# Performance work log

Hardware: AMD Instinct MI355X
Metric: run time of the kernel (lower is better)

The kernel has to match this reference:

```python
import jax, jax.numpy as jnp
import numpy as np

H, B, S, D, T = 4, 16, 2048, 128, 5  # n_head, batch, seq_len, d_model, num event types
BAND_K = 64  # latest-k band width, as in get_latest_k_mask


def setup_inputs() -> dict:
    key = jax.random.key(0)
    ks = jax.random.split(key, 5)
    output = jax.random.normal(ks[0], (B, S, D), dtype=jnp.float32)
    # banded 'latest-k' mask: mask[i, i:i+k] = 1  (start=max(i,i-k+1)=i, end=min(S,i+k))
    i = jnp.arange(S)
    band = ((i[None, :] >= i[:, None]) & (i[None, :] < i[:, None] + BAND_K)).astype(jnp.float32)
    local_cor = band[None]  # [1, S, S]
    cor_matrix = jax.random.normal(ks[1], (T, D), dtype=jnp.float32)
    event_type = jax.random.randint(ks[2], (B, S), 1, T + 1)  # 1-based event ids in [1, T]
    # per-head linear3 params (xavier-ish); self.linear is unused in forward
    W3 = jax.random.normal(ks[3], (H, D, D), dtype=jnp.float32) / np.sqrt(D)
    b3 = jnp.zeros((H, D), dtype=jnp.float32)
    return dict(output=output, local_cor=local_cor, cor_matrix=cor_matrix,
                event_type=event_type, W3=W3, b3=b3)


def reference(output, local_cor, cor_matrix, event_type, W3, b3):
    # (corr^T @ cor_matrix[et-1]).mean(2) == einsum('bsd,bs->bd', corr, cor_matrix[et-1].mean(-1))
    g = cor_matrix.mean(-1)[event_type - 1]  # [B, S]
    x = output
    sum_seq = jnp.zeros_like(output)          # sum over heads of [B,S,D]
    sum_head = jnp.zeros((output.shape[0], output.shape[2]), output.dtype)  # [B,D]
    for h in range(H):
        z = jax.nn.elu(jnp.einsum('bsd,ed->bse', x, W3[h]) + b3[h])  # linear3 + ELU
        corr = jnp.matmul(local_cor, z)       # [1,S,S] @ [B,S,D] -> [B,S,D]
        head_out = jnp.einsum('bsd,bs->bd', corr, g)  # [B,D]
        sum_seq = sum_seq + corr
        sum_head = sum_head + head_out
        x = corr                               # next head consumes correlation_output
    return (sum_seq, sum_head)
```

## Files before the change

kernel.cpp:

```cpp
#include <hip/hip_runtime.h>
#include <math.h>

#define NHEAD 4
#define BATCH 16
#define SEQ   2048
#define DMODEL 128
#define NTYPES 5
#define BAND  64
#define MROWS (BATCH * SEQ)

typedef __attribute__((ext_vector_type(8))) short bf16x8;
typedef __attribute__((ext_vector_type(4))) float f32x4;
typedef __attribute__((ext_vector_type(4))) unsigned int u32x4;

static __device__ __forceinline__ unsigned short f2bf(float f) {
  unsigned int u = __float_as_uint(f);
  unsigned int r = (u + 0x7fffu + ((u >> 16) & 1u)) >> 16;
  return (unsigned short)r;
}
static __device__ __forceinline__ float bflo(unsigned int v) {
  return __uint_as_float(v << 16);
}
static __device__ __forceinline__ float bfhi(unsigned int v) {
  return __uint_as_float(v & 0xffff0000u);
}
static __device__ __forceinline__ unsigned int pkbf(float lo, float hi) {
  return ((unsigned int)f2bf(hi) << 16) | (unsigned int)f2bf(lo);
}
static __device__ __forceinline__ float elu(float v) {
  const float ev = __expf(fminf(v, 0.f)) - 1.f;
  return v > 0.f ? v : ev;
}
static __device__ __forceinline__ int xcd_swz(int blk, int nwg) {
  return (blk & 7) * (nwg >> 3) + (blk >> 3);
}

__global__ __launch_bounds__(512, 4) void gemm0_kernel(
    const float* __restrict__ X0,
    const float* __restrict__ W3,
    const float* __restrict__ bvec,
    unsigned short* __restrict__ Zb,
    float* __restrict__ SH,
    unsigned short* __restrict__ wbf) {
  __shared__ __align__(16) char lds[64 * 272 + 128 * 272];
  char* Xl = lds;
  char* Wl = lds + 64 * 272;
  const int tid = threadIdx.x;
  const int swz = xcd_swz(blockIdx.x, gridDim.x);
  const int row0 = swz * 64;

  if (blockIdx.x < 16 && tid < DMODEL) SH[blockIdx.x * DMODEL + tid] = 0.f;
  if (blockIdx.x < 12) {
    const long u = (long)(blockIdx.x * 512 + tid) * 8 + DMODEL * DMODEL;
    float4 a = *reinterpret_cast<const float4*>(W3 + u);
    float4 c = *reinterpret_cast<const float4*>(W3 + u + 4);
    unsigned short o[8];
    o[0] = f2bf(a.x); o[1] = f2bf(a.y); o[2] = f2bf(a.z); o[3] = f2bf(a.w);
    o[4] = f2bf(c.x); o[5] = f2bf(c.y); o[6] = f2bf(c.z); o[7] = f2bf(c.w);
    *reinterpret_cast<u32x4*>(wbf + u) = *reinterpret_cast<u32x4*>(o);
  }

  #pragma unroll
  for (int it = 0; it < 2; ++it) {
    const int u = it * 512 + tid;
    const int r = u >> 4, g4 = u & 15;
    const float* xs = X0 + (long)(row0 + r) * DMODEL + g4 * 8;
    float4 f0 = *reinterpret_cast<const float4*>(xs);
    float4 f1 = *reinterpret_cast<const float4*>(xs + 4);
    unsigned short o[8];
    o[0] = f2bf(f0.x); o[1] = f2bf(f0.y); o[2] = f2bf(f0.z); o[3] = f2bf(f0.w);
    o[4] = f2bf(f1.x); o[5] = f2bf(f1.y); o[6] = f2bf(f1.z); o[7] = f2bf(f1.w);
    *reinterpret_cast<u32x4*>(Xl + r * 272 + g4 * 16) = *reinterpret_cast<u32x4*>(o);
  }
  #pragma unroll
  for (int it = 0; it < 4; ++it) {
    const int u = it * 512 + tid;
    const int e = u >> 4, g4 = u & 15;
    const float* wsrc = W3 + e * DMODEL + g4 * 8;
    float4 f0 = *reinterpret_cast<const float4*>(wsrc);
    float4 f1 = *reinterpret_cast<const float4*>(wsrc + 4);
    unsigned short o[8];
    o[0] = f2bf(f0.x); o[1] = f2bf(f0.y); o[2] = f2bf(f0.z); o[3] = f2bf(f0.w);
    o[4] = f2bf(f1.x); o[5] = f2bf(f1.y); o[6] = f2bf(f1.z); o[7] = f2bf(f1.w);
    *reinterpret_cast<u32x4*>(Wl + e * 272 + g4 * 16) = *reinterpret_cast<u32x4*>(o);
  }
  __syncthreads();

  const int wv = tid >> 6, l = tid & 63;
  const int mv = wv >> 1, nh = wv & 1;
  const int lr = l & 15, lk = l >> 4;
  f32x4 acc[4];
  #pragma unroll
  for (int n = 0; n < 4; ++n) acc[n] = (f32x4){0.f, 0.f, 0.f, 0.f};
  #pragma unroll
  for (int t = 0; t < 4; ++t) {
    const bf16x8 a = *reinterpret_cast<const bf16x8*>(
        Xl + (mv * 16 + lr) * 272 + (t * 4 + lk) * 16);
    #pragma unroll
    for (int n = 0; n < 4; ++n) {
      const bf16x8 bfrag = *reinterpret_cast<const bf16x8*>(
          Wl + (nh * 64 + n * 16 + lr) * 272 + (t * 4 + lk) * 16);
      acc[n] = __builtin_amdgcn_mfma_f32_16x16x32_bf16(a, bfrag, acc[n], 0, 0, 0);
    }
  }
  #pragma unroll
  for (int n = 0; n < 4; ++n) {
    const int col = nh * 64 + n * 16 + lr;
    const float bias = bvec[col];
    #pragma unroll
    for (int r = 0; r < 4; ++r) {
      const int row = row0 + mv * 16 + lk * 4 + r;
      Zb[(long)row * DMODEL + col] = f2bf(elu(acc[n][r] + bias));
    }
  }
}

template <int ACC>
__global__ __launch_bounds__(512, 4) void fused_band_gemm(
    const unsigned short* __restrict__ Zin,
    const unsigned short* __restrict__ CSin,
    unsigned short* __restrict__ Cout,
    const unsigned short* __restrict__ Wb,
    const float* __restrict__ bvec,
    unsigned short* __restrict__ Zout,
    float* __restrict__ SH,
    const int* __restrict__ et,
    const float* __restrict__ corm) {
  __shared__ __align__(16) char lds[64512];
  char* Xl = lds;
  char* Wl = lds + 17408;
  float2* s8 = reinterpret_cast<float2*>(lds + 52224);
  float* hred = reinterpret_cast<float*>(lds + 60416);
  float* rowmean = reinterpret_cast<float*>(Xl + 256);

  const int tid = threadIdx.x;
  const int swz = xcd_swz(blockIdx.x, gridDim.x);
  const int r0 = swz * 64;
  const int b = r0 >> 11, s0 = r0 & 2047;
  const int p = tid & 63, q = tid >> 6;

  const unsigned int* zsrc =
      reinterpret_cast<const unsigned int*>(Zin) + (long)b * SEQ * 64 + p;
  unsigned int zlo[8], zhi[8];
  int etr[8];
  #pragma unroll
  for (int i = 0; i < 8; ++i) {
    const int sl = s0 + q * 8 + i;
    zlo[i] = zsrc[(long)sl * 64];
    const int sh_ = sl + BAND;
    zhi[i] = (sh_ < SEQ) ? zsrc[(long)sh_ * 64] : 0u;
    etr[i] = et[(long)b * SEQ + sl];
  }
  unsigned int csr[8];
  if (ACC) {
    #pragma unroll
    for (int i = 0; i < 8; ++i)
      csr[i] = *reinterpret_cast<const unsigned int*>(
          CSin + ((long)r0 + q * 8 + i) * DMODEL + 2 * p);
  }
  #pragma unroll
  for (int it = 0; it < 4; ++it) {
    const int u = it * 512 + tid;
    const int e = u >> 4, g4 = u & 15;
    u32x4 v = *reinterpret_cast<const u32x4*>(Wb + e * DMODEL + g4 * 8);
    *reinterpret_cast<u32x4*>(Wl + e * 272 + g4 * 16) = v;
  }
  if (tid < 64) {
    #pragma unroll
    for (int t = 0; t < NTYPES; ++t) {
      float v = corm[t * DMODEL + tid] + corm[t * DMODEL + 64 + tid];
      #pragma unroll
      for (int o = 32; o > 0; o >>= 1) v += __shfl_xor(v, o, 64);
      if (tid == 0) rowmean[t * 68] = v * (1.0f / DMODEL);
    }
  }
  {
    float a0 = 0.f, a1 = 0.f, b0 = 0.f, b1 = 0.f;
    #pragma unroll
    for (int i = 0; i < 8; ++i) {
      a0 += bflo(zlo[i]); a1 += bfhi(zlo[i]);
      b0 += bflo(zhi[i]); b1 += bfhi(zhi[i]);
    }
    s8[q * 64 + p] = make_float2(a0, a1);
    s8[(q + 8) * 64 + p] = make_float2(b0, b1);
  }
  __syncthreads();

  float w0 = 0.f, w1 = 0.f;
  #pragma unroll
  for (int j = 0; j < 8; ++j) {
    const float2 v = s8[(q + j) * 64 + p];
    w0 += v.x; w1 += v.y;
  }
  float hs0 = 0.f, hs1 = 0.f;
  unsigned int pks[8];
  #pragma unroll
  for (int i = 0; i < 8; ++i) {
    const int s = q * 8 + i;
    const float c0v = w0, c1v = w1;
    const float g = rowmean[(etr[i] - 1) * 68];
    hs0 += c0v * g; hs1 += c1v * g;
    const unsigned int raw = pkbf(c0v, c1v);
    if (ACC)
      pks[i] = pkbf(c0v + bflo(csr[i]), c1v + bfhi(csr[i]));
    else
      pks[i] = raw;
    *reinterpret_cast<unsigned int*>(Xl + s * 272 + p * 4) = raw;
    w0 += bflo(zhi[i]) - bflo(zlo[i]);
    w1 += bfhi(zhi[i]) - bfhi(zlo[i]);
  }
  *reinterpret_cast<float2*>(hred + (p * 8 + q) * 2) = make_float2(hs0, hs1);
  __syncthreads();

  #pragma unroll
  for (int i = 0; i < 8; ++i)
    *reinterpret_cast<unsigned int*>(
        Cout + ((long)r0 + q * 8 + i) * DMODEL + 2 * p) = pks[i];
  if (q == 0) {
    float t0 = 0.f, t1 = 0.f;
    #pragma unroll
    for (int k = 0; k < 8; ++k) {
      const float2 v = *reinterpret_cast<const float2*>(hred + (p * 8 + k) * 2);
      t0 += v.x; t1 += v.y;
    }
    atomicAdd(SH + b * DMODEL + 2 * p, t0);
    atomicAdd(SH + b * DMODEL + 2 * p + 1, t1);
  }
  const int wv = tid >> 6, l = tid & 63;
  const int mv = wv >> 1, nh = wv & 1;
  const int lr = l & 15, lk = l >> 4;
  f32x4 acc[4];
  #pragma unroll
  for (int n = 0; n < 4; ++n) acc[n] = (f32x4){0.f, 0.f, 0.f, 0.f};
  #pragma unroll
  for (int t = 0; t < 4; ++t) {
    const bf16x8 a = *reinterpret_cast<const bf16x8*>(
        Xl + (mv * 16 + lr) * 272 + (t * 4 + lk) * 16);
    #pragma unroll
    for (int n = 0; n < 4; ++n) {
      const bf16x8 bfrag = *reinterpret_cast<const bf16x8*>(
          Wl + (nh * 64 + n * 16 + lr) * 272 + (t * 4 + lk) * 16);
      acc[n] = __builtin_amdgcn_mfma_f32_16x16x32_bf16(a, bfrag, acc[n], 0, 0, 0);
    }
  }
  #pragma unroll
  for (int n = 0; n < 4; ++n) {
    const int col = nh * 64 + n * 16 + lr;
    const float bias = bvec[col];
    #pragma unroll
    for (int r = 0; r < 4; ++r) {
      const int row = r0 + mv * 16 + lk * 4 + r;
      Zout[(long)row * DMODEL + col] = f2bf(elu(acc[n][r] + bias));
    }
  }
}

__global__ __launch_bounds__(512, 4) void f2final_kernel(
    const unsigned short* __restrict__ Zin,
    const unsigned short* __restrict__ CSin,
    const unsigned short* __restrict__ Wb,
    const float* __restrict__ bvec,
    float* __restrict__ SS,
    float* __restrict__ SH,
    const int* __restrict__ et,
    const float* __restrict__ corm) {
  __shared__ __align__(16) char lds[71680];
  __shared__ float rowmean[NTYPES];
  char* Xl = lds;
  char* Wl = lds + 34816;
  char* z3 = Wl;
  float2* s8 = reinterpret_cast<float2*>(lds);
  float2* s8v2 = reinterpret_cast<float2*>(lds);
  float* hred = reinterpret_cast<float*>(lds + 69632);

  const int tid = threadIdx.x;
  const int swz = xcd_swz(blockIdx.x, gridDim.x);
  const int r0 = swz * 64;
  const int b = r0 >> 11, s0 = r0 & 2047;
  const int p = tid & 63, q = tid >> 6;

  const unsigned int* zsrc =
      reinterpret_cast<const unsigned int*>(Zin) + (long)b * SEQ * 64 + p;
  unsigned int zlo[16], zhi[16];
  #pragma unroll
  for (int i = 0; i < 16; ++i) {
    const int sl = s0 + q * 16 + i;
    zlo[i] = (sl < SEQ) ? zsrc[(long)sl * 64] : 0u;
    const int sh_ = sl + BAND;
    zhi[i] = (sh_ < SEQ) ? zsrc[(long)sh_ * 64] : 0u;
  }
  unsigned int cs2p[16];
  int etr[16];
  if (q < 4) {
    #pragma unroll
    for (int i = 0; i < 16; ++i) {
      cs2p[i] = *reinterpret_cast<const unsigned int*>(
          CSin + ((long)r0 + q * 16 + i) * DMODEL + 2 * p);
      etr[i] = et[(long)b * SEQ + s0 + q * 16 + i];
    }
  }
  #pragma unroll
  for (int it = 0; it < 4; ++it) {
    const int u = it * 512 + tid;
    const int e = u >> 4, g4 = u & 15;
    u32x4 v = *reinterpret_cast<const u32x4*>(Wb + e * DMODEL + g4 * 8);
    *reinterpret_cast<u32x4*>(Wl + e * 272 + g4 * 16) = v;
  }
  if (tid < 64) {
    #pragma unroll
    for (int t = 0; t < NTYPES; ++t) {
      float v = corm[t * DMODEL + tid] + corm[t * DMODEL + 64 + tid];
      #pragma unroll
      for (int o = 32; o > 0; o >>= 1) v += __shfl_xor(v, o, 64);
      if (tid == 0) rowmean[t] = v * (1.0f / DMODEL);
    }
  }
  {
    float a0 = 0.f, a1 = 0.f, b0 = 0.f, b1 = 0.f;
    #pragma unroll
    for (int i = 0; i < 8; ++i) {
      a0 += bflo(zlo[i]); a1 += bfhi(zlo[i]);
      b0 += bflo(zlo[8 + i]); b1 += bfhi(zlo[8 + i]);
    }
    s8[(2 * q) * 64 + p] = make_float2(a0, a1);
    s8[(2 * q + 1) * 64 + p] = make_float2(b0, b1);
    if (q >= 4) {
      float c0 = 0.f, c1 = 0.f, d0 = 0.f, d1 = 0.f;
      #pragma unroll
      for (int i = 0; i < 8; ++i) {
        c0 += bflo(zhi[i]); c1 += bfhi(zhi[i]);
        d0 += bflo(zhi[8 + i]); d1 += bfhi(zhi[8 + i]);
      }
      s8[(2 * q + 8) * 64 + p] = make_float2(c0, c1);
      s8[(2 * q + 9) * 64 + p] = make_float2(d0, d1);
    }
  }
  __syncthreads();

  float w0 = 0.f, w1 = 0.f;
  #pragma unroll
  for (int j = 0; j < 8; ++j) {
    const float2 v = s8[(2 * q + j) * 64 + p];
    w0 += v.x; w1 += v.y;
  }
  __syncthreads();

  float hs0 = 0.f, hs1 = 0.f;
  #pragma unroll
  for (int i = 0; i < 16; ++i) {
    const int s = q * 16 + i;
    const float c0v = w0, c1v = w1;
    if (q < 4) {
      const float g = rowmean[etr[i] - 1];
      hs0 += c0v * g; hs1 += c1v * g;
      cs2p[i] = pkbf(c0v + bflo(cs2p[i]), c1v + bfhi(cs2p[i]));
    }
    *reinterpret_cast<unsigned int*>(Xl + s * 272 + p * 4) = pkbf(c0v, c1v);
    w0 += bflo(zhi[i]) - bflo(zlo[i]);
    w1 += bfhi(zhi[i]) - bfhi(zlo[i]);
  }
  __syncthreads();

  const int mv = q >> 1, nh = q & 1;
  const int lr = tid & 15, lk = (tid & 63) >> 4;
  f32x4 acc[2][4];
  #pragma unroll
  for (int h2 = 0; h2 < 2; ++h2)
    #pragma unroll
    for (int n = 0; n < 4; ++n) acc[h2][n] = (f32x4){0.f, 0.f, 0.f, 0.f};
  #pragma unroll
  for (int h2 = 0; h2 < 2; ++h2) {
    #pragma unroll
    for (int t = 0; t < 4; ++t) {
      const bf16x8 a = *reinterpret_cast<const bf16x8*>(
          Xl + (h2 * 64 + mv * 16 + lr) * 272 + (t * 4 + lk) * 16);
      #pragma unroll
      for (int n = 0; n < 4; ++n) {
        const bf16x8 bfrag = *reinterpret_cast<const bf16x8*>(
            Wl + (nh * 64 + n * 16 + lr) * 272 + (t * 4 + lk) * 16);
        acc[h2][n] = __builtin_amdgcn_mfma_f32_16x16x32_bf16(a, bfrag,
                                                             acc[h2][n], 0, 0, 0);
      }
    }
  }
  __syncthreads();

  #pragma unroll
  for (int h2 = 0; h2 < 2; ++h2) {
    #pragma unroll
    for (int n = 0; n < 4; ++n) {
      const int col = nh * 64 + n * 16 + lr;
      const float bias = bvec[col];
      #pragma unroll
      for (int r = 0; r < 4; ++r) {
        const int row = h2 * 64 + mv * 16 + lk * 4 + r;
        const float v = elu(acc[h2][n][r] + bias);
        const unsigned short bz =
            (s0 + row < SEQ) ? f2bf(v) : (unsigned short)0;
        *reinterpret_cast<unsigned short*>(z3 + row * 260 + col * 2) = bz;
      }
    }
  }
  __syncthreads();

  {
    float a0 = 0.f, a1 = 0.f, b0 = 0.f, b1 = 0.f;
    #pragma unroll
    for (int jr = 0; jr < 8; ++jr) {
      const unsigned int v0 = *reinterpret_cast<const unsigned int*>(
          z3 + (2 * q * 8 + jr) * 260 + p * 4);
      const unsigned int v1 = *reinterpret_cast<const unsigned int*>(
          z3 + ((2 * q + 1) * 8 + jr) * 260 + p * 4);
      a0 += bflo(v0); a1 += bfhi(v0);
      b0 += bflo(v1); b1 += bfhi(v1);
    }
    s8v2[(2 * q) * 64 + p] = make_float2(a0, a1);
    s8v2[(2 * q + 1) * 64 + p] = make_float2(b0, b1);
  }
  __syncthreads();

  if (q < 4) {
    float v0 = 0.f, v1 = 0.f;
    #pragma unroll
    for (int j = 0; j < 8; ++j) {
      const float2 v = s8v2[(2 * q + j) * 64 + p];
      v0 += v.x; v1 += v.y;
    }
    #pragma unroll
    for (int i = 0; i < 16; ++i) {
      const int s = q * 16 + i;
      const float c3l = v0, c3h = v1;
      const float g = rowmean[etr[i] - 1];
      hs0 += c3l * g; hs1 += c3h * g;
      const float ox = c3l + bflo(cs2p[i]);
      const float oy = c3h + bfhi(cs2p[i]);
      const unsigned long long sv =
          (unsigned long long)__float_as_uint(ox) |
          ((unsigned long long)__float_as_uint(oy) << 32);
      __builtin_nontemporal_store(
          sv, reinterpret_cast<unsigned long long*>(
                  SS + ((long)r0 + s) * DMODEL + 2 * p));
      const unsigned int va = *reinterpret_cast<const unsigned int*>(
          z3 + (s + BAND) * 260 + p * 4);
      const unsigned int vs = *reinterpret_cast<const unsigned int*>(
          z3 + s * 260 + p * 4);
      v0 += bflo(va) - bflo(vs);
      v1 += bfhi(va) - bfhi(vs);
    }
    *reinterpret_cast<float2*>(hred + (p * 4 + q) * 2) = make_float2(hs0, hs1);
  }
  __syncthreads();
  if (q == 0) {
    float t0 = 0.f, t1 = 0.f;
    #pragma unroll
    for (int k = 0; k < 4; ++k) {
      const float2 v = *reinterpret_cast<const float2*>(hred + (p * 4 + k) * 2);
      t0 += v.x; t1 += v.y;
    }
    atomicAdd(SH + b * DMODEL + 2 * p, t0);
    atomicAdd(SH + b * DMODEL + 2 * p + 1, t1);
  }
}

extern "C" void kernel_launch(void* const* d_in, const int* in_sizes, int n_in,
                              void* d_out, int out_size, void* d_ws, size_t ws_size,
                              hipStream_t stream) {
  const float* x0   = (const float*)d_in[0];
  const float* corm = (const float*)d_in[2];
  const int*   et   = (const int*)d_in[3];
  const float* W3   = (const float*)d_in[4];
  const float* b3   = (const float*)d_in[5];

  float* out_ss = (float*)d_out;
  float* out_sh = out_ss + (size_t)MROWS * DMODEL;

  char* ws = (char*)d_ws;
  const size_t MB = 1024 * 1024;
  unsigned short* A = (unsigned short*)(ws + 0 * MB);
  unsigned short* B = (unsigned short*)(ws + 8 * MB);
  unsigned short* C = (unsigned short*)(ws + 16 * MB);
  unsigned short* E = (unsigned short*)(ws + 24 * MB);
  unsigned short* wbf = (unsigned short*)(ws + 32 * MB);

  const size_t WSTR = (size_t)DMODEL * DMODEL;

  gemm0_kernel<<<512, 512, 0, stream>>>(x0, W3, b3, A, out_sh, wbf);
  fused_band_gemm<0><<<512, 512, 0, stream>>>(
      A, nullptr, B, wbf + 1 * WSTR, b3 + 1 * DMODEL, E, out_sh, et, corm);
  fused_band_gemm<1><<<512, 512, 0, stream>>>(
      E, B, C, wbf + 2 * WSTR, b3 + 2 * DMODEL, A, out_sh, et, corm);
  f2final_kernel<<<512, 512, 0, stream>>>(
      A, C, wbf + 3 * WSTR, b3 + 3 * DMODEL, out_ss, out_sh, et, corm);
}
```

Measured before the change: 51.92 us.

## Fuse two band-GEMM head stages into one kernel with halo recompute

Merges the two per-head band-sum + linear+ELU kernels into a single kernel. Each block loads a 128-row window (64 output rows plus a 64-row halo) and recomputes the intermediate head's Z for the halo in LDS. This removes one launch and the global round trip of the intermediate Z and corr buffers. In exchange the first GEMM is done twice per block, LDS use and register pressure go up, and only half the waves work in some phases.

```diff
diff --git a/kernel.cpp b/kernel.cpp
--- a/kernel.cpp
+++ b/kernel.cpp
@@ -115,23 +115,25 @@
   }
 }
 
-template <int ACC>
-__global__ __launch_bounds__(512, 4) void fused_band_gemm(
+__global__ __launch_bounds__(512, 4) void f01_kernel(
     const unsigned short* __restrict__ Zin,
-    const unsigned short* __restrict__ CSin,
-    unsigned short* __restrict__ Cout,
-    const unsigned short* __restrict__ Wb,
-    const float* __restrict__ bvec,
-    unsigned short* __restrict__ Zout,
+    const unsigned short* __restrict__ W1b,
+    const float* __restrict__ b1,
+    const unsigned short* __restrict__ W2b,
+    const float* __restrict__ b2,
+    unsigned short* __restrict__ CS1,
+    unsigned short* __restrict__ Z2,
     float* __restrict__ SH,
     const int* __restrict__ et,
     const float* __restrict__ corm) {
-  __shared__ __align__(16) char lds[64512];
+  __shared__ __align__(16) char lds[71680];
+  __shared__ float rowmean[NTYPES];
   char* Xl = lds;
-  char* Wl = lds + 17408;
-  float2* s8 = reinterpret_cast<float2*>(lds + 52224);
-  float* hred = reinterpret_cast<float*>(lds + 60416);
-  float* rowmean = reinterpret_cast<float*>(Xl + 256);
+  char* Wl = lds + 34816;
+  char* z1 = Wl;
+  float2* s8 = reinterpret_cast<float2*>(lds);
+  float2* s8v2 = reinterpret_cast<float2*>(lds + 17408);
+  float* hred = reinterpret_cast<float*>(lds + 69632);
 
   const int tid = threadIdx.x;
   const int swz = xcd_swz(blockIdx.x, gridDim.x);
@@ -141,28 +143,26 @@
 
   const unsigned int* zsrc =
       reinterpret_cast<const unsigned int*>(Zin) + (long)b * SEQ * 64 + p;
-  unsigned int zlo[8], zhi[8];
-  int etr[8];
-  #pragma unroll
-  for (int i = 0; i < 8; ++i) {
-    const int sl = s0 + q * 8 + i;
-    zlo[i] = zsrc[(long)sl * 64];
+  unsigned int zlo[16], zhi[16];
+  #pragma unroll
+  for (int i = 0; i < 16; ++i) {
+    const int sl = s0 + q * 16 + i;
+    zlo[i] = (sl < SEQ) ? zsrc[(long)sl * 64] : 0u;
     const int sh_ = sl + BAND;
     zhi[i] = (sh_ < SEQ) ? zsrc[(long)sh_ * 64] : 0u;
-    etr[i] = et[(long)b * SEQ + sl];
-  }
-  unsigned int csr[8];
-  if (ACC) {
-    #pragma unroll
-    for (int i = 0; i < 8; ++i)
-      csr[i] = *reinterpret_cast<const unsigned int*>(
-          CSin + ((long)r0 + q * 8 + i) * DMODEL + 2 * p);
+  }
+  unsigned int c0p[16];
+  int etr[16];
+  if (q < 4) {
+    #pragma unroll
+    for (int i = 0; i < 16; ++i)
+      etr[i] = et[(long)b * SEQ + s0 + q * 16 + i];
   }
   #pragma unroll
   for (int it = 0; it < 4; ++it) {
     const int u = it * 512 + tid;
     const int e = u >> 4, g4 = u & 15;
-    u32x4 v = *reinterpret_cast<const u32x4*>(Wb + e * DMODEL + g4 * 8);
+    u32x4 v = *reinterpret_cast<const u32x4*>(W1b + e * DMODEL + g4 * 8);
     *reinterpret_cast<u32x4*>(Wl + e * 272 + g4 * 16) = v;
   }
   if (tid < 64) {
@@ -171,86 +171,192 @@
       float v = corm[t * DMODEL + tid] + corm[t * DMODEL + 64 + tid];
       #pragma unroll
       for (int o = 32; o > 0; o >>= 1) v += __shfl_xor(v, o, 64);
-      if (tid == 0) rowmean[t * 68] = v * (1.0f / DMODEL);
+      if (tid == 0) rowmean[t] = v * (1.0f / DMODEL);
     }
   }
   {
-    float a0 = 0.f, a1 = 0.f, b0 = 0.f, b1 = 0.f;
+    float a0 = 0.f, a1 = 0.f, b0 = 0.f, b1v = 0.f;
     #pragma unroll
     for (int i = 0; i < 8; ++i) {
       a0 += bflo(zlo[i]); a1 += bfhi(zlo[i]);
-      b0 += bflo(zhi[i]); b1 += bfhi(zhi[i]);
-    }
-    s8[q * 64 + p] = make_float2(a0, a1);
-    s8[(q + 8) * 64 + p] = make_float2(b0, b1);
+      b0 += bflo(zlo[8 + i]); b1v += bfhi(zlo[8 + i]);
+    }
+    s8[(2 * q) * 64 + p] = make_float2(a0, a1);
+    s8[(2 * q + 1) * 64 + p] = make_float2(b0, b1v);
+    if (q >= 4) {
+      float c0 = 0.f, c1 = 0.f, d0 = 0.f, d1 = 0.f;
+      #pragma unroll
+      for (int i = 0; i < 8; ++i) {
+        c0 += bflo(zhi[i]); c1 += bfhi(zhi[i]);
+        d0 += bflo(zhi[8 + i]); d1 += bfhi(zhi[8 + i]);
+      }
+      s8[(2 * q + 8) * 64 + p] = make_float2(c0, c1);
+      s8[(2 * q + 9) * 64 + p] = make_float2(d0, d1);
+    }
   }
   __syncthreads();
 
   float w0 = 0.f, w1 = 0.f;
   #pragma unroll
   for (int j = 0; j < 8; ++j) {
-    const float2 v = s8[(q + j) * 64 + p];
+    const float2 v = s8[(2 * q + j) * 64 + p];
     w0 += v.x; w1 += v.y;
   }
+  __syncthreads();
+
   float hs0 = 0.f, hs1 = 0.f;
-  unsigned int pks[8];
-  #pragma unroll
-  for (int i = 0; i < 8; ++i) {
-    const int s = q * 8 + i;
+  #pragma unroll
+  for (int i = 0; i < 16; ++i) {
+    const int s = q * 16 + i;
     const float c0v = w0, c1v = w1;
-    const float g = rowmean[(etr[i] - 1) * 68];
-    hs0 += c0v * g; hs1 += c1v * g;
     const unsigned int raw = pkbf(c0v, c1v);
-    if (ACC)
-      pks[i] = pkbf(c0v + bflo(csr[i]), c1v + bfhi(csr[i]));
-    else
-      pks[i] = raw;
+    if (q < 4) {
+      const float g = rowmean[etr[i] - 1];
+      hs0 += c0v * g; hs1 += c1v * g;
+      c0p[i] = raw;
+    }
     *reinterpret_cast<unsigned int*>(Xl + s * 272 + p * 4) = raw;
     w0 += bflo(zhi[i]) - bflo(zlo[i]);
     w1 += bfhi(zhi[i]) - bfhi(zlo[i]);
   }
-  *reinterpret_cast<float2*>(hred + (p * 8 + q) * 2) = make_float2(hs0, hs1);
-  __syncthreads();
-
-  #pragma unroll
-  for (int i = 0; i < 8; ++i)
-    *reinterpret_cast<unsigned int*>(
-        Cout + ((long)r0 + q * 8 + i) * DMODEL + 2 * p) = pks[i];
+  __syncthreads();
+
+  const int mv = q >> 1, nh = q & 1;
+  const int lr = tid & 15, lk = (tid & 63) >> 4;
+  f32x4 acc[2][4];
+  #pragma unroll
+  for (int h2 = 0; h2 < 2; ++h2)
+    #pragma unroll
+    for (int n = 0; n < 4; ++n) acc[h2][n] = (f32x4){0.f, 0.f, 0.f, 0.f};
+  #pragma unroll
+  for (int h2 = 0; h2 < 2; ++h2) {
+    #pragma unroll
+    for (int t = 0; t < 4; ++t) {
+      const bf16x8 a = *reinterpret_cast<const bf16x8*>(
+          Xl + (h2 * 64 + mv * 16 + lr) * 272 + (t * 4 + lk) * 16);
+      #pragma unroll
+      for (int n = 0; n < 4; ++n) {
+        const bf16x8 bfrag = *reinterpret_cast<const bf16x8*>(
+            Wl + (nh * 64 + n * 16 + lr) * 272 + (t * 4 + lk) * 16);
+        acc[h2][n] = __builtin_amdgcn_mfma_f32_16x16x32_bf16(a, bfrag,
+                                                             acc[h2][n], 0, 0, 0);
+      }
+    }
+  }
+  __syncthreads();
+
+  #pragma unroll
+  for (int h2 = 0; h2 < 2; ++h2) {
+    #pragma unroll
+    for (int n = 0; n < 4; ++n) {
+      const int col = nh * 64 + n * 16 + lr;
+      const float bias = b1[col];
+      #pragma unroll
+      for (int r = 0; r < 4; ++r) {
+        const int row = h2 * 64 + mv * 16 + lk * 4 + r;
+        const float v = elu(acc[h2][n][r] + bias);
+        const unsigned short bz =
+            (s0 + row < SEQ) ? f2bf(v) : (unsigned short)0;
+        *reinterpret_cast<unsigned short*>(z1 + row * 260 + col * 2) = bz;
+      }
+    }
+  }
+  __syncthreads();
+
+  {
+    float a0 = 0.f, a1 = 0.f, b0 = 0.f, b1v = 0.f;
+    #pragma unroll
+    for (int jr = 0; jr < 8; ++jr) {
+      const unsigned int v0 = *reinterpret_cast<const unsigned int*>(
+          z1 + (2 * q * 8 + jr) * 260 + p * 4);
+      const unsigned int v1 = *reinterpret_cast<const unsigned int*>(
+          z1 + ((2 * q + 1) * 8 + jr) * 260 + p * 4);
+      a0 += bflo(v0); a1 += bfhi(v0);
+      b0 += bflo(v1); b1v += bfhi(v1);
+    }
+    s8v2[(2 * q) * 64 + p] = make_float2(a0, a1);
+    s8v2[(2 * q + 1) * 64 + p] = make_float2(b0, b1v);
+  }
+  __syncthreads();
+
+  if (q < 4) {
+    float v0 = 0.f, v1 = 0.f;
+    #pragma unroll
+    for (int j = 0; j < 8; ++j) {
+      const float2 v = s8v2[(2 * q + j) * 64 + p];
+      v0 += v.x; v1 += v.y;
+    }
+    #pragma unroll
+    for (int i = 0; i < 16; ++i) {
+      const int s = q * 16 + i;
+      const float c1l = v0, c1h = v1;
+      const float g = rowmean[etr[i] - 1];
+      hs0 += c1l * g; hs1 += c1h * g;
+      *reinterpret_cast<unsigned int*>(Xl + s * 272 + p * 4) = pkbf(c1l, c1h);
+      c0p[i] = pkbf(c1l + bflo(c0p[i]), c1h + bfhi(c0p[i]));
+      const unsigned int va = *reinterpret_cast<const unsigned int*>(
+          z1 + (s + BAND) * 260 + p * 4);
+      const unsigned int vs = *reinterpret_cast<const unsigned int*>(
+          z1 + s * 260 + p * 4);
+      v0 += bflo(va) - bflo(vs);
+      v1 += bfhi(va) - bfhi(vs);
+    }
+    *reinterpret_cast<float2*>(hred + (p * 4 + q) * 2) = make_float2(hs0, hs1);
+  }
+  __syncthreads();
+
+  #pragma unroll
+  for (int it = 0; it < 4; ++it) {
+    const int u = it * 512 + tid;
+    const int e = u >> 4, g4 = u & 15;
+    u32x4 v = *reinterpret_cast<const u32x4*>(W2b + e * DMODEL + g4 * 8);
+    *reinterpret_cast<u32x4*>(Wl + e * 272 + g4 * 16) = v;
+  }
+  if (q < 4) {
+    #pragma unroll
+    for (int i = 0; i < 16; ++i)
+      *reinterpret_cast<unsigned int*>(
+          CS1 + ((long)r0 + q * 16 + i) * DMODEL + 2 * p) = c0p[i];
+  }
   if (q == 0) {
     float t0 = 0.f, t1 = 0.f;
     #pragma unroll
-    for (int k = 0; k < 8; ++k) {
-      const float2 v = *reinterpret_cast<const float2*>(hred + (p * 8 + k) * 2);
+    for (int k = 0; k < 4; ++k) {
+      const float2 v = *reinterpret_cast<const float2*>(hred + (p * 4 + k) * 2);
       t0 += v.x; t1 += v.y;
     }
     atomicAdd(SH + b * DMODEL + 2 * p, t0);
     atomicAdd(SH + b * DMODEL + 2 * p + 1, t1);
   }
-  const int wv = tid >> 6, l = tid & 63;
-  const int mv = wv >> 1, nh = wv & 1;
-  const int lr = l & 15, lk = l >> 4;
-  f32x4 acc[4];
-  #pragma unroll
-  for (int n = 0; n < 4; ++n) acc[n] = (f32x4){0.f, 0.f, 0.f, 0.f};
-  #pragma unroll
-  for (int t = 0; t < 4; ++t) {
-    const bf16x8 a = *reinterpret_cast<const bf16x8*>(
-        Xl + (mv * 16 + lr) * 272 + (t * 4 + lk) * 16);
+  __syncthreads();
+
+  {
+    const int wv = tid >> 6;
+    const int mv2 = wv >> 1, nh2 = wv & 1;
+    f32x4 acc2[4];
+    #pragma unroll
+    for (int n = 0; n < 4; ++n) acc2[n] = (f32x4){0.f, 0.f, 0.f, 0.f};
+    #pragma unroll
+    for (int t = 0; t < 4; ++t) {
+      const bf16x8 a = *reinterpret_cast<const bf16x8*>(
+          Xl + (mv2 * 16 + lr) * 272 + (t * 4 + lk) * 16);
+      #pragma unroll
+      for (int n = 0; n < 4; ++n) {
+        const bf16x8 bfrag = *reinterpret_cast<const bf16x8*>(
+            Wl + (nh2 * 64 + n * 16 + lr) * 272 + (t * 4 + lk) * 16);
+        acc2[n] = __builtin_amdgcn_mfma_f32_16x16x32_bf16(a, bfrag, acc2[n],
+                                                          0, 0, 0);
+      }
+    }
     #pragma unroll
     for (int n = 0; n < 4; ++n) {
-      const bf16x8 bfrag = *reinterpret_cast<const bf16x8*>(
-          Wl + (nh * 64 + n * 16 + lr) * 272 + (t * 4 + lk) * 16);
-      acc[n] = __builtin_amdgcn_mfma_f32_16x16x32_bf16(a, bfrag, acc[n], 0, 0, 0);
-    }
-  }
-  #pragma unroll
-  for (int n = 0; n < 4; ++n) {
-    const int col = nh * 64 + n * 16 + lr;
-    const float bias = bvec[col];
-    #pragma unroll
-    for (int r = 0; r < 4; ++r) {
-      const int row = r0 + mv * 16 + lk * 4 + r;
-      Zout[(long)row * DMODEL + col] = f2bf(elu(acc[n][r] + bias));
+      const int col = nh2 * 64 + n * 16 + lr;
+      const float bias = b2[col];
+      #pragma unroll
+      for (int r = 0; r < 4; ++r) {
+        const int row = r0 + mv2 * 16 + lk * 4 + r;
+        Z2[(long)row * DMODEL + col] = f2bf(elu(acc2[n][r] + bias));
+      }
     }
   }
 }
@@ -477,18 +583,16 @@
   char* ws = (char*)d_ws;
   const size_t MB = 1024 * 1024;
   unsigned short* A = (unsigned short*)(ws + 0 * MB);
-  unsigned short* B = (unsigned short*)(ws + 8 * MB);
-  unsigned short* C = (unsigned short*)(ws + 16 * MB);
-  unsigned short* E = (unsigned short*)(ws + 24 * MB);
-  unsigned short* wbf = (unsigned short*)(ws + 32 * MB);
+  unsigned short* C = (unsigned short*)(ws + 8 * MB);
+  unsigned short* D = (unsigned short*)(ws + 16 * MB);
+  unsigned short* wbf = (unsigned short*)(ws + 24 * MB);
 
   const size_t WSTR = (size_t)DMODEL * DMODEL;
 
   gemm0_kernel<<<512, 512, 0, stream>>>(x0, W3, b3, A, out_sh, wbf);
-  fused_band_gemm<0><<<512, 512, 0, stream>>>(
-      A, nullptr, B, wbf + 1 * WSTR, b3 + 1 * DMODEL, E, out_sh, et, corm);
-  fused_band_gemm<1><<<512, 512, 0, stream>>>(
-      E, B, C, wbf + 2 * WSTR, b3 + 2 * DMODEL, A, out_sh, et, corm);
+  f01_kernel<<<512, 512, 0, stream>>>(
+      A, wbf + 1 * WSTR, b3 + 1 * DMODEL, wbf + 2 * WSTR, b3 + 2 * DMODEL,
+      C, D, out_sh, et, corm);
   f2final_kernel<<<512, 512, 0, stream>>>(
-      A, C, wbf + 3 * WSTR, b3 + 3 * DMODEL, out_ss, out_sh, et, corm);
-}
+      D, C, wbf + 3 * WSTR, b3 + 3 * DMODEL, out_ss, out_sh, et, corm);
+}
```

Result: slower. 53.44 us (+2.9%).
